# Kernel tuning notes

Measured on AMD Instinct MI355X. Metric: run time of the kernel, lower is better.

## Reference

```python
import jax, jax.numpy as jnp
import numpy as np

EMB_DIM = 1024
NUM_HEADS = 16
HEAD_DIM = EMB_DIM // NUM_HEADS


def setup_inputs() -> dict:
    key = jax.random.key(0)
    ks = jax.random.split(key, 6)
    B, S, D = 2, 2048, EMB_DIM
    x = jax.random.normal(ks[0], (B, S, D), dtype=jnp.float32)
    # torch nn.Linear default init: U(-1/sqrt(in), 1/sqrt(in)); weights stored [out,in]
    lim = 1.0 / np.sqrt(D)
    Wq = jax.random.uniform(ks[1], (D, D), jnp.float32, -lim, lim)
    Wk = jax.random.uniform(ks[2], (D, D), jnp.float32, -lim, lim)
    Wv = jax.random.uniform(ks[3], (D, D), jnp.float32, -lim, lim)
    Wo = jax.random.uniform(ks[4], (D, D), jnp.float32, -lim, lim)
    q_scale = jnp.ones((1, 1, D), jnp.float32)
    k_scale = jnp.ones((1, 1, D), jnp.float32)
    v_scale = jnp.ones((1, 1, D), jnp.float32)
    o_scale = jnp.ones((1, 1, D), jnp.float32)
    return {"x": x, "Wq": Wq, "Wk": Wk, "Wv": Wv, "Wo": Wo,
            "q_scale": q_scale, "k_scale": k_scale,
            "v_scale": v_scale, "o_scale": o_scale}


def reference(x, Wq, Wk, Wv, Wo, q_scale, k_scale, v_scale, o_scale):
    B, S, D = x.shape
    H, Hd = NUM_HEADS, HEAD_DIM
    # linear (torch: x @ W^T) then per-channel scale
    Q = (x @ Wq.T) * q_scale
    K = (x @ Wk.T) * k_scale
    V = (x @ Wv.T) * v_scale
    # [B, H, S, Hd]
    Q = Q.reshape(B, S, H, Hd).transpose(0, 2, 1, 3)
    K = K.reshape(B, S, H, Hd).transpose(0, 2, 1, 3)
    V = V.reshape(B, S, H, Hd).transpose(0, 2, 1, 3)
    scores = jnp.einsum("bhqd,bhkd->bhqk", Q, K) / jnp.sqrt(
        jnp.asarray(Hd, jnp.float32))
    probs = jax.nn.softmax(scores, axis=-1)
    ctx = jnp.einsum("bhqk,bhkd->bhqd", probs, V)
    ctx = ctx.transpose(0, 2, 1, 3).reshape(B, S, D)
    return (ctx @ Wo.T) * o_scale
```

## Files before the change

kernel.cpp:

```cpp
#include <hip/hip_runtime.h>
#include <hip/hip_bf16.h>
#include <stdint.h>


typedef __bf16 bf16;
typedef __attribute__((ext_vector_type(8))) __bf16 bf16x8;
typedef __attribute__((ext_vector_type(4))) float f32x4;

#define DEVI __device__ __forceinline__

DEVI bf16x8 load8(const bf16* p) { return *(const bf16x8*)p; }
DEVI bf16x8 load8(const float* p) {
  f32x4 a = *(const f32x4*)p;
  f32x4 b = *(const f32x4*)(p + 4);
  bf16x8 r;
  r[0] = (bf16)a[0]; r[1] = (bf16)a[1]; r[2] = (bf16)a[2]; r[3] = (bf16)a[3];
  r[4] = (bf16)b[0]; r[5] = (bf16)b[1]; r[6] = (bf16)b[2]; r[7] = (bf16)b[3];
  return r;
}

template <typename XT, int NTILE>
__global__ __launch_bounds__(256, 2)
void gemm_kernel(const XT* __restrict__ X,
                 const float* __restrict__ W0, const float* __restrict__ W1,
                 const float* __restrict__ W2,
                 const float* __restrict__ s0, const float* __restrict__ s1,
                 const float* __restrict__ s2,
                 bf16* __restrict__ o0, bf16* __restrict__ o1,
                 bf16* __restrict__ o2, float* __restrict__ ofp, int three) {
  constexpr int NF = NTILE / 32;
  __shared__ bf16 As[128 * 32];
  __shared__ bf16 Bs[NTILE * 32];

  const int t = threadIdx.x;
  const int lane = t & 63;
  const int w = t >> 6;
  const int wm = (NTILE == 128) ? (w >> 1) : (w >> 1);
  const int wn = w & 1;
  const int m0 = blockIdx.x * 128;
  const int cl = lane & 15, quad = lane >> 4;

  const float* Wp; const float* sp; bf16* op; int mode, n0; float emul = 1.f;
  if (three) {
    int which = blockIdx.y >> 3;
    n0 = (blockIdx.y & 7) * 128;
    if (which == 0)      { Wp = W0; sp = s0; op = o0; mode = 1; emul = 0.18033688f; }
    else if (which == 1) { Wp = W1; sp = s1; op = o1; mode = 1; }
    else                 { Wp = W2; sp = s2; op = o2; mode = 2; }
  } else {
    n0 = blockIdx.y * NTILE; Wp = W0; sp = s0; op = o0; mode = 0;
  }

  f32x4 zero = {0.f, 0.f, 0.f, 0.f};
  f32x4 acc[4][NF];
#pragma unroll
  for (int i = 0; i < 4; i++)
#pragma unroll
    for (int j = 0; j < NF; j++) acc[i][j] = zero;

  const int srow = t >> 2;
  const int gcol = (t & 3) * 8;
  const int sphys = (((t & 3) ^ (srow & 3)) << 3);

  for (int k0 = 0; k0 < 1024; k0 += 32) {
    bf16x8 a0 = load8(&X[(uint64_t)(m0 + srow)      * 1024 + k0 + gcol]);
    bf16x8 a1 = load8(&X[(uint64_t)(m0 + 64 + srow) * 1024 + k0 + gcol]);
    bf16x8 b0 = load8(&Wp[(uint64_t)(n0 + srow)      * 1024 + k0 + gcol]);
    bf16x8 b1;
    if (NTILE == 128)
      b1 = load8(&Wp[(uint64_t)(n0 + 64 + srow) * 1024 + k0 + gcol]);
    __syncthreads();
    *(bf16x8*)&As[srow * 32 + sphys]        = a0;
    *(bf16x8*)&As[(64 + srow) * 32 + sphys] = a1;
    *(bf16x8*)&Bs[srow * 32 + sphys]        = b0;
    if (NTILE == 128)
      *(bf16x8*)&Bs[(64 + srow) * 32 + sphys] = b1;
    __syncthreads();

    bf16x8 af[4], bfr[NF];
#pragma unroll
    for (int mt = 0; mt < 4; mt++) {
      const int row = wm * 64 + mt * 16 + cl;
      af[mt] = *(const bf16x8*)&As[row * 32 + ((quad ^ (cl & 3)) << 3)];
    }
#pragma unroll
    for (int nt = 0; nt < NF; nt++) {
      const int row = wn * (NF * 16) + nt * 16 + cl;
      bfr[nt] = *(const bf16x8*)&Bs[row * 32 + ((quad ^ (cl & 3)) << 3)];
    }
#pragma unroll
    for (int mt = 0; mt < 4; mt++)
#pragma unroll
      for (int nt = 0; nt < NF; nt++)
        acc[mt][nt] = __builtin_amdgcn_mfma_f32_16x16x32_bf16(af[mt], bfr[nt],
                                                              acc[mt][nt], 0, 0, 0);
  }

#pragma unroll
  for (int nt = 0; nt < NF; nt++) {
    const int gn = n0 + wn * (NF * 16) + nt * 16 + cl;
    const float sc = sp[gn] * emul;
#pragma unroll
    for (int mt = 0; mt < 4; mt++) {
      const int gmb = m0 + wm * 64 + mt * 16 + quad * 4;
#pragma unroll
      for (int r = 0; r < 4; r++) {
        const int gm = gmb + r;
        const float v = acc[mt][nt][r] * sc;
        if (mode == 0) {
          ofp[(uint64_t)gm * 1024 + gn] = v;
        } else {
          const int b = gm >> 11, s = gm & 2047;
          const int h = gn >> 6, hd = gn & 63;
          uint64_t addr;
          if (mode == 1) addr = ((uint64_t)(b * 16 + h) * 2048 + s) * 64 + hd;
          else           addr = ((uint64_t)(b * 16 + h) * 64 + hd) * 2048 + s;
          op[addr] = (bf16)v;
        }
      }
    }
  }
}

__global__ __launch_bounds__(256, 2)
void attn_kernel(const bf16* __restrict__ Qw, const bf16* __restrict__ Kw,
                 const bf16* __restrict__ Vtw, bf16* __restrict__ Ctx) {
  __shared__ bf16 Ks[64 * 64];
  __shared__ bf16 Vs[64 * 64];
  __shared__ bf16 Ps[8 * 16 * 64];

  const int t = threadIdx.x, lane = t & 63, w = t >> 6;
  const int cl = lane & 15, quad = lane >> 4;
  const int bh = blockIdx.y;
  const int b = bh >> 4, h = bh & 15;
  const int q0 = blockIdx.x * 128;

  const bf16* Qh = Qw + (uint64_t)bh * 2048 * 64;
  const bf16* Kh = Kw + (uint64_t)bh * 2048 * 64;
  const bf16* Vh = Vtw + (uint64_t)bh * 64 * 2048;

  bf16x8 qf[2][2];
#pragma unroll
  for (int mt = 0; mt < 2; mt++) {
    const int r = q0 + mt * 64 + w * 16 + cl;
    qf[mt][0] = *(const bf16x8*)&Qh[(uint64_t)r * 64 + quad * 8];
    qf[mt][1] = *(const bf16x8*)&Qh[(uint64_t)r * 64 + 32 + quad * 8];
  }

  f32x4 zero = {0.f, 0.f, 0.f, 0.f};
  f32x4 o_acc[2][4];
  float lsum[2][4];
#pragma unroll
  for (int mt = 0; mt < 2; mt++)
#pragma unroll
    for (int i = 0; i < 4; i++) { o_acc[mt][i] = zero; lsum[mt][i & 3] = 0.f; }

  const int srow = t >> 3;
  const int gcol = (t & 7) * 8;
  const int sphys = (((t & 7) ^ (srow & 7)) << 3);

  for (int k0 = 0; k0 < 2048; k0 += 64) {
    bf16x8 kv0 = *(const bf16x8*)&Kh[(uint64_t)(k0 + srow) * 64 + gcol];
    bf16x8 kv1 = *(const bf16x8*)&Kh[(uint64_t)(k0 + 32 + srow) * 64 + gcol];
    bf16x8 vv0 = *(const bf16x8*)&Vh[(uint64_t)srow * 2048 + k0 + gcol];
    bf16x8 vv1 = *(const bf16x8*)&Vh[(uint64_t)(32 + srow) * 2048 + k0 + gcol];
    __syncthreads();
    *(bf16x8*)&Ks[srow * 64 + sphys]        = kv0;
    *(bf16x8*)&Ks[(32 + srow) * 64 + sphys] = kv1;
    *(bf16x8*)&Vs[srow * 64 + sphys]        = vv0;
    *(bf16x8*)&Vs[(32 + srow) * 64 + sphys] = vv1;
    __syncthreads();

    f32x4 sv[2][4];
#pragma unroll
    for (int nt = 0; nt < 4; nt++) {
      const int krow = nt * 16 + cl;
      bf16x8 kf0 = *(const bf16x8*)&Ks[krow * 64 + ((quad ^ (cl & 7)) << 3)];
      bf16x8 kf1 = *(const bf16x8*)&Ks[krow * 64 + (((quad + 4) ^ (cl & 7)) << 3)];
#pragma unroll
      for (int mt = 0; mt < 2; mt++) {
        f32x4 s = __builtin_amdgcn_mfma_f32_16x16x32_bf16(qf[mt][0], kf0, zero, 0, 0, 0);
        s = __builtin_amdgcn_mfma_f32_16x16x32_bf16(qf[mt][1], kf1, s, 0, 0, 0);
        sv[mt][nt] = s;
      }
    }

#pragma unroll
    for (int mt = 0; mt < 2; mt++) {
      bf16* Pm = Ps + (w * 2 + mt) * 1024;
#pragma unroll
      for (int nt = 0; nt < 4; nt++) {
#pragma unroll
        for (int r = 0; r < 4; r++) {
          const float p = __builtin_amdgcn_exp2f(sv[mt][nt][r]);
          lsum[mt][r] += p;
          const int row = quad * 4 + r;
          Pm[row * 64 + ((((nt * 2 + (cl >> 3)) ^ (row & 7)) << 3) | (cl & 7))] =
              (bf16)p;
        }
      }
    }

    bf16x8 pf[2][2];
#pragma unroll
    for (int mt = 0; mt < 2; mt++) {
      const bf16* Pm = Ps + (w * 2 + mt) * 1024;
      pf[mt][0] = *(const bf16x8*)&Pm[cl * 64 + ((quad ^ (cl & 7)) << 3)];
      pf[mt][1] = *(const bf16x8*)&Pm[cl * 64 + (((quad + 4) ^ (cl & 7)) << 3)];
    }
#pragma unroll
    for (int nt = 0; nt < 4; nt++) {
      const int vrow = nt * 16 + cl;
      bf16x8 v0 = *(const bf16x8*)&Vs[vrow * 64 + ((quad ^ (cl & 7)) << 3)];
      bf16x8 v1 = *(const bf16x8*)&Vs[vrow * 64 + (((quad + 4) ^ (cl & 7)) << 3)];
#pragma unroll
      for (int mt = 0; mt < 2; mt++) {
        o_acc[mt][nt] = __builtin_amdgcn_mfma_f32_16x16x32_bf16(pf[mt][0], v0,
                                                                o_acc[mt][nt], 0, 0, 0);
        o_acc[mt][nt] = __builtin_amdgcn_mfma_f32_16x16x32_bf16(pf[mt][1], v1,
                                                                o_acc[mt][nt], 0, 0, 0);
      }
    }
  }

  float linv[2][4];
#pragma unroll
  for (int mt = 0; mt < 2; mt++)
#pragma unroll
    for (int r = 0; r < 4; r++) {
      float l = lsum[mt][r];
      l += __shfl_xor(l, 1);
      l += __shfl_xor(l, 2);
      l += __shfl_xor(l, 4);
      l += __shfl_xor(l, 8);
      linv[mt][r] = 1.0f / l;
    }
#pragma unroll
  for (int mt = 0; mt < 2; mt++)
#pragma unroll
    for (int nt = 0; nt < 4; nt++)
#pragma unroll
      for (int r = 0; r < 4; r++) {
        const int s = q0 + mt * 64 + w * 16 + quad * 4 + r;
        const int hd = nt * 16 + cl;
        Ctx[(uint64_t)(b * 2048 + s) * 1024 + h * 64 + hd] =
            (bf16)(o_acc[mt][nt][r] * linv[mt][r]);
      }
}

extern "C" void kernel_launch(void* const* d_in, const int* in_sizes, int n_in,
                              void* d_out, int out_size, void* d_ws, size_t ws_size,
                              hipStream_t stream) {
  const float* x  = (const float*)d_in[0];
  const float* Wq = (const float*)d_in[1];
  const float* Wk = (const float*)d_in[2];
  const float* Wv = (const float*)d_in[3];
  const float* Wo = (const float*)d_in[4];
  const float* qs = (const float*)d_in[5];
  const float* ks = (const float*)d_in[6];
  const float* vs = (const float*)d_in[7];
  const float* os = (const float*)d_in[8];
  float* out = (float*)d_out;

  bf16* qw = (bf16*)d_ws;
  bf16* kw = qw + (size_t)4096 * 1024;
  bf16* vw = kw + (size_t)4096 * 1024;
  bf16* cw = vw + (size_t)4096 * 1024;

  gemm_kernel<float, 128><<<dim3(32, 24), 256, 0, stream>>>(
      x, Wq, Wk, Wv, qs, ks, vs, qw, kw, vw, nullptr, 1);
  attn_kernel<<<dim3(16, 32), 256, 0, stream>>>(qw, kw, vw, cw);
  gemm_kernel<bf16, 64><<<dim3(32, 16), 256, 0, stream>>>(
      cw, Wo, nullptr, nullptr, os, nullptr, nullptr,
      nullptr, nullptr, nullptr, out, 0);
}
```

Before: 221.0 us.

## Pre-convert inputs to bf16, use direct global-to-LDS loads, enlarge attention tile

Adds a conversion kernel that casts x and all four weight matrices to bf16 in workspace, so the GEMMs can stage tiles with global_load_lds straight into LDS instead of loading fp32 and converting in registers. The attention kernel also loads K/V through direct-to-LDS loads and doubles the query tile per block to 256 rows, with occupancy lowered to one block. This trades an extra conversion pass and lower occupancy, with half as many attention blocks, for fewer register round-trips and more K/V reuse. A fallback path keeps the old fp32 loads when the workspace is too small.

Measured after the change: 221.1 us. No clear change (+0.1%).

```diff
diff --git a/kernel.cpp b/kernel.cpp
--- a/kernel.cpp
+++ b/kernel.cpp
@@ -8,6 +8,12 @@
 typedef __attribute__((ext_vector_type(4))) float f32x4;
 
 #define DEVI __device__ __forceinline__
+
+DEVI void gl_lds16(const void* g, void* l) {
+  __builtin_amdgcn_global_load_lds(
+      (const __attribute__((address_space(1))) void*)g,
+      (__attribute__((address_space(3))) void*)l, 16, 0, 0);
+}
 
 DEVI bf16x8 load8(const bf16* p) { return *(const bf16x8*)p; }
 DEVI bf16x8 load8(const float* p) {
@@ -19,28 +25,48 @@
   return r;
 }
 
-template <typename XT, int NTILE>
+__global__ __launch_bounds__(256)
+void cvt_kernel(const float* __restrict__ x,
+                const float* __restrict__ w0, const float* __restrict__ w1,
+                const float* __restrict__ w2, const float* __restrict__ w3,
+                bf16* __restrict__ xb, bf16* __restrict__ wb) {
+  const int y = blockIdx.y;
+  const float* src;
+  bf16* dst;
+  if (y < 4) {
+    src = (y == 0) ? w0 : (y == 1) ? w1 : (y == 2) ? w2 : w3;
+    dst = wb + (size_t)y * 1048576;
+  } else {
+    src = x + (size_t)(y - 4) * 1048576;
+    dst = xb + (size_t)(y - 4) * 1048576;
+  }
+  const int i = (blockIdx.x * 256 + threadIdx.x) * 8;
+  *(bf16x8*)(dst + i) = load8(src + i);
+}
+
+template <typename XT, typename WT, int NTILE>
 __global__ __launch_bounds__(256, 2)
 void gemm_kernel(const XT* __restrict__ X,
-                 const float* __restrict__ W0, const float* __restrict__ W1,
-                 const float* __restrict__ W2,
+                 const WT* __restrict__ W0, const WT* __restrict__ W1,
+                 const WT* __restrict__ W2,
                  const float* __restrict__ s0, const float* __restrict__ s1,
                  const float* __restrict__ s2,
                  bf16* __restrict__ o0, bf16* __restrict__ o1,
                  bf16* __restrict__ o2, float* __restrict__ ofp, int three) {
   constexpr int NF = NTILE / 32;
+  constexpr bool ASYNC_A = (sizeof(XT) == 2);
+  constexpr bool ASYNC_B = (sizeof(WT) == 2);
   __shared__ bf16 As[128 * 32];
   __shared__ bf16 Bs[NTILE * 32];
 
   const int t = threadIdx.x;
   const int lane = t & 63;
   const int w = t >> 6;
-  const int wm = (NTILE == 128) ? (w >> 1) : (w >> 1);
-  const int wn = w & 1;
+  const int wm = w >> 1, wn = w & 1;
   const int m0 = blockIdx.x * 128;
   const int cl = lane & 15, quad = lane >> 4;
 
-  const float* Wp; const float* sp; bf16* op; int mode, n0; float emul = 1.f;
+  const WT* Wp; const float* sp; bf16* op; int mode, n0; float emul = 1.f;
   if (three) {
     int which = blockIdx.y >> 3;
     n0 = (blockIdx.y & 7) * 128;
@@ -59,22 +85,41 @@
     for (int j = 0; j < NF; j++) acc[i][j] = zero;
 
   const int srow = t >> 2;
+  const int clog = (t & 3) ^ (srow & 3);
+  const int gcol_sw = clog * 8;
   const int gcol = (t & 3) * 8;
   const int sphys = (((t & 3) ^ (srow & 3)) << 3);
 
   for (int k0 = 0; k0 < 1024; k0 += 32) {
-    bf16x8 a0 = load8(&X[(uint64_t)(m0 + srow)      * 1024 + k0 + gcol]);
-    bf16x8 a1 = load8(&X[(uint64_t)(m0 + 64 + srow) * 1024 + k0 + gcol]);
-    bf16x8 b0 = load8(&Wp[(uint64_t)(n0 + srow)      * 1024 + k0 + gcol]);
-    bf16x8 b1;
-    if (NTILE == 128)
-      b1 = load8(&Wp[(uint64_t)(n0 + 64 + srow) * 1024 + k0 + gcol]);
+    bf16x8 a0, a1, b0, b1;
+    if constexpr (!ASYNC_A) {
+      a0 = load8(&X[(uint64_t)(m0 + srow) * 1024 + k0 + gcol]);
+      a1 = load8(&X[(uint64_t)(m0 + 64 + srow) * 1024 + k0 + gcol]);
+    }
+    if constexpr (!ASYNC_B) {
+      b0 = load8(&Wp[(uint64_t)(n0 + srow) * 1024 + k0 + gcol]);
+      if constexpr (NTILE == 128)
+        b1 = load8(&Wp[(uint64_t)(n0 + 64 + srow) * 1024 + k0 + gcol]);
+    }
     __syncthreads();
-    *(bf16x8*)&As[srow * 32 + sphys]        = a0;
-    *(bf16x8*)&As[(64 + srow) * 32 + sphys] = a1;
-    *(bf16x8*)&Bs[srow * 32 + sphys]        = b0;
-    if (NTILE == 128)
-      *(bf16x8*)&Bs[(64 + srow) * 32 + sphys] = b1;
+    if constexpr (ASYNC_A) {
+      gl_lds16(X + (uint64_t)(m0 + srow) * 1024 + k0 + gcol_sw, (char*)As + t * 16);
+      gl_lds16(X + (uint64_t)(m0 + 64 + srow) * 1024 + k0 + gcol_sw,
+               (char*)As + 4096 + t * 16);
+    } else {
+      *(bf16x8*)&As[srow * 32 + sphys] = a0;
+      *(bf16x8*)&As[(64 + srow) * 32 + sphys] = a1;
+    }
+    if constexpr (ASYNC_B) {
+      gl_lds16(Wp + (uint64_t)(n0 + srow) * 1024 + k0 + gcol_sw, (char*)Bs + t * 16);
+      if constexpr (NTILE == 128)
+        gl_lds16(Wp + (uint64_t)(n0 + 64 + srow) * 1024 + k0 + gcol_sw,
+                 (char*)Bs + 4096 + t * 16);
+    } else {
+      *(bf16x8*)&Bs[srow * 32 + sphys] = b0;
+      if constexpr (NTILE == 128)
+        *(bf16x8*)&Bs[(64 + srow) * 32 + sphys] = b1;
+    }
     __syncthreads();
 
     bf16x8 af[4], bfr[NF];
@@ -122,63 +167,58 @@
   }
 }
 
-__global__ __launch_bounds__(256, 2)
+__global__ __launch_bounds__(256, 1)
 void attn_kernel(const bf16* __restrict__ Qw, const bf16* __restrict__ Kw,
                  const bf16* __restrict__ Vtw, bf16* __restrict__ Ctx) {
   __shared__ bf16 Ks[64 * 64];
   __shared__ bf16 Vs[64 * 64];
-  __shared__ bf16 Ps[8 * 16 * 64];
+  __shared__ bf16 Ps[16 * 16 * 64];
 
   const int t = threadIdx.x, lane = t & 63, w = t >> 6;
   const int cl = lane & 15, quad = lane >> 4;
   const int bh = blockIdx.y;
   const int b = bh >> 4, h = bh & 15;
-  const int q0 = blockIdx.x * 128;
+  const int q0 = blockIdx.x * 256;
 
   const bf16* Qh = Qw + (uint64_t)bh * 2048 * 64;
   const bf16* Kh = Kw + (uint64_t)bh * 2048 * 64;
   const bf16* Vh = Vtw + (uint64_t)bh * 64 * 2048;
 
-  bf16x8 qf[2][2];
-#pragma unroll
-  for (int mt = 0; mt < 2; mt++) {
+  bf16x8 qf[4][2];
+#pragma unroll
+  for (int mt = 0; mt < 4; mt++) {
     const int r = q0 + mt * 64 + w * 16 + cl;
     qf[mt][0] = *(const bf16x8*)&Qh[(uint64_t)r * 64 + quad * 8];
     qf[mt][1] = *(const bf16x8*)&Qh[(uint64_t)r * 64 + 32 + quad * 8];
   }
 
   f32x4 zero = {0.f, 0.f, 0.f, 0.f};
-  f32x4 o_acc[2][4];
-  float lsum[2][4];
-#pragma unroll
-  for (int mt = 0; mt < 2; mt++)
-#pragma unroll
-    for (int i = 0; i < 4; i++) { o_acc[mt][i] = zero; lsum[mt][i & 3] = 0.f; }
+  f32x4 o_acc[4][4];
+  float lsum[4][4];
+#pragma unroll
+  for (int mt = 0; mt < 4; mt++)
+#pragma unroll
+    for (int i = 0; i < 4; i++) { o_acc[mt][i] = zero; lsum[mt][i] = 0.f; }
 
   const int srow = t >> 3;
-  const int gcol = (t & 7) * 8;
-  const int sphys = (((t & 7) ^ (srow & 7)) << 3);
+  const int gcol_sw = ((t & 7) ^ (srow & 7)) * 8;
 
   for (int k0 = 0; k0 < 2048; k0 += 64) {
-    bf16x8 kv0 = *(const bf16x8*)&Kh[(uint64_t)(k0 + srow) * 64 + gcol];
-    bf16x8 kv1 = *(const bf16x8*)&Kh[(uint64_t)(k0 + 32 + srow) * 64 + gcol];
-    bf16x8 vv0 = *(const bf16x8*)&Vh[(uint64_t)srow * 2048 + k0 + gcol];
-    bf16x8 vv1 = *(const bf16x8*)&Vh[(uint64_t)(32 + srow) * 2048 + k0 + gcol];
     __syncthreads();
-    *(bf16x8*)&Ks[srow * 64 + sphys]        = kv0;
-    *(bf16x8*)&Ks[(32 + srow) * 64 + sphys] = kv1;
-    *(bf16x8*)&Vs[srow * 64 + sphys]        = vv0;
-    *(bf16x8*)&Vs[(32 + srow) * 64 + sphys] = vv1;
+    gl_lds16(Kh + (uint64_t)(k0 + srow) * 64 + gcol_sw,        (char*)Ks + t * 16);
+    gl_lds16(Kh + (uint64_t)(k0 + 32 + srow) * 64 + gcol_sw,   (char*)Ks + 4096 + t * 16);
+    gl_lds16(Vh + (uint64_t)srow * 2048 + k0 + gcol_sw,        (char*)Vs + t * 16);
+    gl_lds16(Vh + (uint64_t)(32 + srow) * 2048 + k0 + gcol_sw, (char*)Vs + 4096 + t * 16);
     __syncthreads();
 
-    f32x4 sv[2][4];
+    f32x4 sv[4][4];
 #pragma unroll
     for (int nt = 0; nt < 4; nt++) {
       const int krow = nt * 16 + cl;
       bf16x8 kf0 = *(const bf16x8*)&Ks[krow * 64 + ((quad ^ (cl & 7)) << 3)];
       bf16x8 kf1 = *(const bf16x8*)&Ks[krow * 64 + (((quad + 4) ^ (cl & 7)) << 3)];
 #pragma unroll
-      for (int mt = 0; mt < 2; mt++) {
+      for (int mt = 0; mt < 4; mt++) {
         f32x4 s = __builtin_amdgcn_mfma_f32_16x16x32_bf16(qf[mt][0], kf0, zero, 0, 0, 0);
         s = __builtin_amdgcn_mfma_f32_16x16x32_bf16(qf[mt][1], kf1, s, 0, 0, 0);
         sv[mt][nt] = s;
@@ -186,8 +226,8 @@
     }
 
 #pragma unroll
-    for (int mt = 0; mt < 2; mt++) {
-      bf16* Pm = Ps + (w * 2 + mt) * 1024;
+    for (int mt = 0; mt < 4; mt++) {
+      bf16* Pm = Ps + (w * 4 + mt) * 1024;
 #pragma unroll
       for (int nt = 0; nt < 4; nt++) {
 #pragma unroll
@@ -201,10 +241,10 @@
       }
     }
 
-    bf16x8 pf[2][2];
-#pragma unroll
-    for (int mt = 0; mt < 2; mt++) {
-      const bf16* Pm = Ps + (w * 2 + mt) * 1024;
+    bf16x8 pf[4][2];
+#pragma unroll
+    for (int mt = 0; mt < 4; mt++) {
+      const bf16* Pm = Ps + (w * 4 + mt) * 1024;
       pf[mt][0] = *(const bf16x8*)&Pm[cl * 64 + ((quad ^ (cl & 7)) << 3)];
       pf[mt][1] = *(const bf16x8*)&Pm[cl * 64 + (((quad + 4) ^ (cl & 7)) << 3)];
     }
@@ -214,7 +254,7 @@
       bf16x8 v0 = *(const bf16x8*)&Vs[vrow * 64 + ((quad ^ (cl & 7)) << 3)];
       bf16x8 v1 = *(const bf16x8*)&Vs[vrow * 64 + (((quad + 4) ^ (cl & 7)) << 3)];
 #pragma unroll
-      for (int mt = 0; mt < 2; mt++) {
+      for (int mt = 0; mt < 4; mt++) {
         o_acc[mt][nt] = __builtin_amdgcn_mfma_f32_16x16x32_bf16(pf[mt][0], v0,
                                                                 o_acc[mt][nt], 0, 0, 0);
         o_acc[mt][nt] = __builtin_amdgcn_mfma_f32_16x16x32_bf16(pf[mt][1], v1,
@@ -223,9 +263,8 @@
     }
   }
 
-  float linv[2][4];
-#pragma unroll
-  for (int mt = 0; mt < 2; mt++)
+#pragma unroll
+  for (int mt = 0; mt < 4; mt++)
 #pragma unroll
     for (int r = 0; r < 4; r++) {
       float l = lsum[mt][r];
@@ -233,10 +272,10 @@
       l += __shfl_xor(l, 2);
       l += __shfl_xor(l, 4);
       l += __shfl_xor(l, 8);
-      linv[mt][r] = 1.0f / l;
-    }
-#pragma unroll
-  for (int mt = 0; mt < 2; mt++)
+      lsum[mt][r] = 1.0f / l;
+    }
+#pragma unroll
+  for (int mt = 0; mt < 4; mt++)
 #pragma unroll
     for (int nt = 0; nt < 4; nt++)
 #pragma unroll
@@ -244,7 +283,7 @@
         const int s = q0 + mt * 64 + w * 16 + quad * 4 + r;
         const int hd = nt * 16 + cl;
         Ctx[(uint64_t)(b * 2048 + s) * 1024 + h * 64 + hd] =
-            (bf16)(o_acc[mt][nt][r] * linv[mt][r]);
+            (bf16)(o_acc[mt][nt][r] * lsum[mt][r]);
       }
 }
 
@@ -262,15 +301,33 @@
   const float* os = (const float*)d_in[8];
   float* out = (float*)d_out;
 
-  bf16* qw = (bf16*)d_ws;
-  bf16* kw = qw + (size_t)4096 * 1024;
-  bf16* vw = kw + (size_t)4096 * 1024;
-  bf16* cw = vw + (size_t)4096 * 1024;
-
-  gemm_kernel<float, 128><<<dim3(32, 24), 256, 0, stream>>>(
-      x, Wq, Wk, Wv, qs, ks, vs, qw, kw, vw, nullptr, 1);
-  attn_kernel<<<dim3(16, 32), 256, 0, stream>>>(qw, kw, vw, cw);
-  gemm_kernel<bf16, 64><<<dim3(32, 16), 256, 0, stream>>>(
-      cw, Wo, nullptr, nullptr, os, nullptr, nullptr,
-      nullptr, nullptr, nullptr, out, 0);
-}
+  const size_t M4 = 4194304, M1 = 1048576;
+
+  if (ws_size >= (size_t)40 * 1024 * 1024) {
+    bf16* xb = (bf16*)d_ws;
+    bf16* wb = xb + M4;
+    bf16* qw = wb + M4;
+    bf16* kw = qw + M4;
+    bf16* vw = kw + M4;
+    bf16* cw = xb;
+
+    cvt_kernel<<<dim3(512, 8), 256, 0, stream>>>(x, Wq, Wk, Wv, Wo, xb, wb);
+    gemm_kernel<bf16, bf16, 128><<<dim3(32, 24), 256, 0, stream>>>(
+        xb, wb, wb + M1, wb + 2 * M1, qs, ks, vs, qw, kw, vw, nullptr, 1);
+    attn_kernel<<<dim3(8, 32), 256, 0, stream>>>(qw, kw, vw, cw);
+    gemm_kernel<bf16, bf16, 64><<<dim3(32, 16), 256, 0, stream>>>(
+        cw, wb + 3 * M1, nullptr, nullptr, os, nullptr, nullptr,
+        nullptr, nullptr, nullptr, out, 0);
+  } else {
+    bf16* qw = (bf16*)d_ws;
+    bf16* kw = qw + M4;
+    bf16* vw = kw + M4;
+    bf16* cw = vw + M4;
+    gemm_kernel<float, float, 128><<<dim3(32, 24), 256, 0, stream>>>(
+        x, Wq, Wk, Wv, qs, ks, vs, qw, kw, vw, nullptr, 1);
+    attn_kernel<<<dim3(8, 32), 256, 0, stream>>>(qw, kw, vw, cw);
+    gemm_kernel<bf16, float, 64><<<dim3(32, 16), 256, 0, stream>>>(
+        cw, Wo, nullptr, nullptr, os, nullptr, nullptr,
+        nullptr, nullptr, nullptr, out, 0);
+  }
+}
```
